# Performance work log

Measured on AMD Instinct MI355X. Metric: run time of the kernel, lower is better.

## Reference

```python
import jax, jax.numpy as jnp
import numpy as np

B, N, D, H, DH, M = 4, 4096, 1024, 16, 64, 256
EPS = 1e-4


def softmax_kernel(data, P, is_query):
    # data: [b,h,n,dh], P: [m,dh]  (FAVOR+ positive softmax features)
    dn = data.shape[-1] ** -0.25
    ratio = P.shape[0] ** -0.5
    dd = jnp.einsum('bhnd,md->bhnm', dn * data, P)
    diag = (jnp.sum(data * data, axis=-1) * 0.5 * dn * dn)[..., None]  # [b,h,n,1]
    if is_query:
        mx = jnp.max(dd, axis=-1, keepdims=True)  # per-query max
    else:
        mx = jnp.max(dd)  # global max (as in torch source)
    return ratio * (jnp.exp(dd - diag - mx) + EPS)


def setup_inputs() -> dict:
    key = jax.random.key(0)
    ks = jax.random.split(key, 6)
    s = 1.0 / np.sqrt(D).astype(np.float32)
    x = jax.random.normal(ks[0], (B, N, D), jnp.float32)
    Wq = jax.random.normal(ks[1], (D, H * DH), jnp.float32) * s
    Wk = jax.random.normal(ks[2], (D, H * DH), jnp.float32) * s
    Wv = jax.random.normal(ks[3], (D, H * DH), jnp.float32) * s
    Wo = jax.random.normal(ks[4], (H * DH, D), jnp.float32) * s
    bo = jnp.zeros((D,), jnp.float32)
    P = jax.random.normal(ks[5], (M, DH), jnp.float32)  # gaussian (orthogonal) projection
    return {'x': x, 'Wq': Wq, 'Wk': Wk, 'Wv': Wv, 'Wo': Wo, 'bo': bo, 'P': P}


def reference(x, Wq, Wk, Wv, Wo, bo, P):
    b, n, _ = x.shape
    # qkv projections, split heads: b n (h d) -> b h n d
    def proj(W):
        return (x @ W).reshape(b, n, H, DH).transpose(0, 2, 1, 3)
    q, k, v = proj(Wq), proj(Wk), proj(Wv)
    qp = softmax_kernel(q, P, is_query=True)   # [b,h,n,m]
    kp = softmax_kernel(k, P, is_query=False)  # [b,h,n,m]
    # linear attention (Performer)
    k_cumsum = kp.sum(axis=-2)                                   # [b,h,m]
    D_inv = 1.0 / jnp.einsum('bhnm,bhm->bhn', qp, k_cumsum)      # [b,h,n]
    ctx = jnp.einsum('bhnm,bhne->bhme', kp, v)                   # [b,h,m,dh]
    out = jnp.einsum('bhme,bhnm,bhn->bhne', ctx, qp, D_inv)      # [b,h,n,dh]
    out = out.transpose(0, 2, 1, 3).reshape(b, n, H * DH)
    return out @ Wo + bo
```

## Files before the change

### kernel.cpp

```cpp
#include <hip/hip_runtime.h>
#include <math.h>

#define NB 4
#define NSEQ 4096
#define DM 1024
#define NHEAD 16
#define DHD 64
#define MF 256
#define ROWS 16384

#define DN 0.35355339059327373f
#define RATIO 0.0625f
#define HALF_DN2 0.0625f
#define EPSF 1.0e-4f
#define THR_DEFER 4.0f

typedef __attribute__((ext_vector_type(4))) float f32x4;
typedef __attribute__((ext_vector_type(8))) short short8;
typedef __attribute__((ext_vector_type(4))) short short4v;
typedef __attribute__((ext_vector_type(8))) __bf16 bf16x8;
typedef unsigned short ushort_t;

__device__ __forceinline__ unsigned short f2bf(float f) {
  unsigned int u = __builtin_bit_cast(unsigned int, f);
  u += 0x7FFFu + ((u >> 16) & 1u);
  return (unsigned short)(u >> 16);
}
__device__ __forceinline__ float bf2f(unsigned short h) {
  unsigned int u = ((unsigned int)h) << 16;
  return __builtin_bit_cast(float, u);
}

__device__ __forceinline__ f32x4 mfma16(short8 a, short8 b, f32x4 c) {
  return __builtin_amdgcn_mfma_f32_16x16x32_bf16(
      __builtin_bit_cast(bf16x8, a), __builtin_bit_cast(bf16x8, b), c, 0, 0, 0);
}

__device__ __forceinline__ f32x4 mfma16x16(short4v a, short4v b, f32x4 c) {
#if __has_builtin(__builtin_amdgcn_mfma_f32_16x16x16bf16_1k)
  return __builtin_amdgcn_mfma_f32_16x16x16bf16_1k(a, b, c, 0, 0, 0);
#elif __has_builtin(__builtin_amdgcn_mfma_f32_16x16x16_bf16)
  typedef __attribute__((ext_vector_type(4))) __bf16 bf16x4;
  return __builtin_amdgcn_mfma_f32_16x16x16_bf16(
      __builtin_bit_cast(bf16x4, a), __builtin_bit_cast(bf16x4, b), c, 0, 0, 0);
#else
  asm volatile("s_nop 1\n\t"
               "v_mfma_f32_16x16x16_bf16 %0, %1, %2, %0\n\t"
               "s_nop 7"
               : "+v"(c) : "v"(a), "v"(b));
  return c;
#endif
}

__device__ __forceinline__ void glds16(const void* g, void* l) {
  __builtin_amdgcn_global_load_lds(
      (const __attribute__((address_space(1))) unsigned int*)g,
      (__attribute__((address_space(3))) unsigned int*)l, 16, 0, 0);
}

__global__ __launch_bounds__(256) void wtrans(const float* __restrict__ W,
                                              ushort_t* __restrict__ Wt)
{
  __shared__ float ts[64][68];
  const int tid = threadIdx.x;
  const int k0 = blockIdx.y * 64, n0 = blockIdx.x * 64;
  const int r = tid >> 4, c4 = (tid & 15) * 4;
  #pragma unroll
  for (int i = 0; i < 4; ++i) {
    float4 v = *(const float4*)&W[(size_t)(k0 + r + i * 16) * DM + n0 + c4];
    *(float4*)&ts[r + i * 16][c4] = v;
  }
  __syncthreads();
  #pragma unroll
  for (int i = 0; i < 4; ++i) {
    const int n = r + i * 16;
    ushort4 o;
    o.x = f2bf(ts[c4 + 0][n]); o.y = f2bf(ts[c4 + 1][n]);
    o.z = f2bf(ts[c4 + 2][n]); o.w = f2bf(ts[c4 + 3][n]);
    *(ushort4*)&Wt[(size_t)(n0 + n) * DM + k0 + c4] = o;
  }
}

__global__ __launch_bounds__(256) void psplit(const float* __restrict__ P,
                                              ushort_t* __restrict__ PHI,
                                              ushort_t* __restrict__ PLO)
{
  const int i = blockIdx.x * 256 + threadIdx.x;
  const float v = P[i];
  const unsigned short h = f2bf(v);
  PHI[i] = h;
  PLO[i] = f2bf(v - bf2f(h));
}

__global__ __launch_bounds__(256) void xconv(const float* __restrict__ x,
                                             ushort_t* __restrict__ xb)
{
  const size_t i = ((size_t)blockIdx.x * 256 + threadIdx.x) * 8;
  const float4 a = *(const float4*)&x[i];
  const float4 c = *(const float4*)&x[i + 4];
  short8 o;
  o[0] = f2bf(a.x); o[1] = f2bf(a.y); o[2] = f2bf(a.z); o[3] = f2bf(a.w);
  o[4] = f2bf(c.x); o[5] = f2bf(c.y); o[6] = f2bf(c.z); o[7] = f2bf(c.w);
  *(short8*)&xb[i] = o;
}

template<int EPI>
__global__ __launch_bounds__(256) void gemm_k(const ushort_t* __restrict__ Ab,
                                              const ushort_t* __restrict__ Bt,
                                              const float* __restrict__ bias,
                                              float* __restrict__ C,
                                              ushort_t* __restrict__ VT,
                                              ushort_t* __restrict__ OHL,
                                              float* __restrict__ DIAG)
{
  constexpr int K = DM, N = DM;
  __shared__ ushort_t As[128 * 32];
  __shared__ ushort_t Bs[128 * 32];

  const int tid = threadIdx.x;
  const int l = tid & 63, w = tid >> 6;
  const int ll = l & 15, lh = l >> 4;
  const int wr = w >> 1, wc = w & 1;

  const int bid = blockIdx.x;
  const int swz = (bid & 7) * ((int)gridDim.x >> 3) + (bid >> 3);
  const int bm = swz >> 3, bn = swz & 7;
  const int row0 = bm * 128, col0 = bn * 128;

  const int pb0 = w * 128 + l, pb1 = pb0 + 64;
  const int brow0 = pb0 >> 2, bkq0 = (pb0 & 3) ^ ((brow0 >> 1) & 3);
  const int brow1 = pb1 >> 2, bkq1 = (pb1 & 3) ^ ((brow1 >> 1) & 3);
  const ushort_t* bsrc0 = Bt + (size_t)(col0 + brow0) * K + bkq0 * 8;
  const ushort_t* bsrc1 = Bt + (size_t)(col0 + brow1) * K + bkq1 * 8;
  ushort_t* bdst0 = &Bs[(size_t)(w * 128) * 8];
  ushort_t* bdst1 = &Bs[(size_t)(w * 128 + 64) * 8];

  const ushort_t* asrc0 = Ab + (size_t)(row0 + brow0) * K + bkq0 * 8;
  const ushort_t* asrc1 = Ab + (size_t)(row0 + brow1) * K + bkq1 * 8;

  int aoff[4], boff[4];
  #pragma unroll
  for (int mt = 0; mt < 4; ++mt) {
    const int r = wr * 64 + mt * 16 + ll;
    aoff[mt] = (r * 4 + (lh ^ ((r >> 1) & 3))) * 8;
  }
  #pragma unroll
  for (int nt = 0; nt < 4; ++nt) {
    const int r = wc * 64 + nt * 16 + ll;
    boff[nt] = (r * 4 + (lh ^ ((r >> 1) & 3))) * 8;
  }

  f32x4 acc[4][4];
  #pragma unroll
  for (int i = 0; i < 4; ++i)
    #pragma unroll
    for (int j = 0; j < 4; ++j) acc[i][j] = (f32x4){0.f, 0.f, 0.f, 0.f};

  for (int k0 = 0; k0 < K; k0 += 32) {
    __syncthreads();
    glds16(asrc0 + k0, &As[(size_t)(w * 128) * 8]);
    glds16(asrc1 + k0, &As[(size_t)(w * 128 + 64) * 8]);
    glds16(bsrc0 + k0, bdst0);
    glds16(bsrc1 + k0, bdst1);
    __syncthreads();

    short8 av[4], bv[4];
    #pragma unroll
    for (int mt = 0; mt < 4; ++mt) av[mt] = *(const short8*)&As[aoff[mt]];
    #pragma unroll
    for (int nt = 0; nt < 4; ++nt) bv[nt] = *(const short8*)&Bs[boff[nt]];
    #pragma unroll
    for (int mt = 0; mt < 4; ++mt)
      #pragma unroll
      for (int nt = 0; nt < 4; ++nt)
        acc[mt][nt] = mfma16(av[mt], bv[nt], acc[mt][nt]);
  }

  if constexpr (EPI == 1) {
    #pragma unroll
    for (int mt = 0; mt < 4; ++mt) {
      #pragma unroll
      for (int nt = 0; nt < 4; ++nt) {
        const int row = row0 + wr * 64 + mt * 16 + lh * 4;
        const int col = col0 + wc * 64 + nt * 16 + ll;
        const float bv_ = bias[col];
        #pragma unroll
        for (int j = 0; j < 4; ++j)
          C[(size_t)(row + j) * N + col] = acc[mt][nt][j] + bv_;
      }
    }
  } else if constexpr (EPI == 2) {
    #pragma unroll
    for (int mt = 0; mt < 4; ++mt) {
      #pragma unroll
      for (int nt = 0; nt < 4; ++nt) {
        const int rg = row0 + wr * 64 + mt * 16 + lh * 4;
        const int cg = col0 + wc * 64 + nt * 16 + ll;
        const int b = rg >> 12, n = rg & 4095;
        const int h = cg >> 6, dh = cg & 63;
        ushort4 o;
        o.x = f2bf(acc[mt][nt][0]); o.y = f2bf(acc[mt][nt][1]);
        o.z = f2bf(acc[mt][nt][2]); o.w = f2bf(acc[mt][nt][3]);
        *(ushort4*)&VT[(((size_t)b * 16 + h) * 64 + dh) * 4096 + n] = o;
      }
    }
  } else {
    const int hglob = (col0 >> 6) + wc;
    #pragma unroll
    for (int mt = 0; mt < 4; ++mt) {
      float rssq[4] = {0.f, 0.f, 0.f, 0.f};
      #pragma unroll
      for (int nt = 0; nt < 4; ++nt) {
        const int row = row0 + wr * 64 + mt * 16 + lh * 4;
        const int e = nt * 16 + ll;
        #pragma unroll
        for (int j = 0; j < 4; ++j) {
          const float v = acc[mt][nt][j];
          rssq[j] += v * v;
          const unsigned short hh = f2bf(v);
          const size_t base = ((size_t)(row + j) * 16 + hglob) * 128 + e;
          OHL[base] = hh;
          OHL[base + 64] = f2bf(v - bf2f(hh));
        }
      }
      #pragma unroll
      for (int j = 0; j < 4; ++j) {
        float s = rssq[j];
        s += __shfl_xor(s, 1, 64); s += __shfl_xor(s, 2, 64);
        s += __shfl_xor(s, 4, 64); s += __shfl_xor(s, 8, 64);
        if (ll == 0) {
          const int row = row0 + wr * 64 + mt * 16 + lh * 4 + j;
          DIAG[(((row >> 12) * 16 + hglob) << 12) + (row & 4095)] = HALF_DN2 * s;
        }
      }
    }
  }
}

__global__ __launch_bounds__(256, 4) void kside6(const ushort_t* __restrict__ KHL,
                                                 const ushort_t* __restrict__ VT,
                                                 const ushort_t* __restrict__ PHI,
                                                 const ushort_t* __restrict__ PLO,
                                                 const float* __restrict__ DIAGK,
                                                 float* __restrict__ partC,
                                                 float* __restrict__ partK,
                                                 float* __restrict__ mw,
                                                 float* __restrict__ vsum,
                                                 unsigned* __restrict__ mxp)
{
  const int tid = threadIdx.x;
  const int l = tid & 63, mg = tid >> 6;
  const int ll = l & 15, lh = l >> 4;
  const int blk = blockIdx.x;
  const int bh = blk >> 4, ck = (blk >> 1) & 7, mh = blk & 1;
  const int b = bh >> 4, h = bh & 15;
  const int mbase = mh * 128 + mg * 32;

  short8 pfh[2][2], pfl[2][2];
  #pragma unroll
  for (int mt = 0; mt < 2; ++mt)
    #pragma unroll
    for (int ks = 0; ks < 2; ++ks) {
      const size_t off = (size_t)(mbase + mt * 16 + ll) * 64 + ks * 32 + lh * 8;
      pfh[mt][ks] = *(const short8*)&PHI[off];
      pfl[mt][ks] = *(const short8*)&PLO[off];
    }

  f32x4 apv[2][4];
  #pragma unroll
  for (int i = 0; i < 2; ++i)
    #pragma unroll
    for (int j = 0; j < 4; ++j) apv[i][j] = (f32x4){0.f, 0.f, 0.f, 0.f};
  float kcp[2] = {0.f, 0.f};
  float vs[4] = {0.f, 0.f, 0.f, 0.f};
  float m_run = -1.0e30f, tmax = -1.0e30f;

  const int n0 = ck * 512;
  const ushort_t* krow = KHL + ((size_t)(b * NSEQ + n0 + ll) * 16 + h) * 128 + lh * 8;
  const ushort_t* vrow = VT + (size_t)bh * 64 * NSEQ + n0 + lh * 4;
  const float* drow = DIAGK + bh * 4096 + n0 + lh * 4;

  for (int it = 0; it < 32; ++it) {
    const ushort_t* kp_ = krow + (size_t)it * 16 * 2048;
    const short8 kh0 = *(const short8*)(kp_);
    const short8 kh1 = *(const short8*)(kp_ + 32);
    const short8 kl0 = *(const short8*)(kp_ + 64);
    const short8 kl1 = *(const short8*)(kp_ + 96);
    const float4 dg4 = *(const float4*)(drow + it * 16);
    short4v vf[4];
    #pragma unroll
    for (int dt = 0; dt < 4; ++dt)
      vf[dt] = *(const short4v*)&vrow[(size_t)(dt * 16 + ll) * NSEQ + it * 16];

    f32x4 dda[2];
    #pragma unroll
    for (int mt = 0; mt < 2; ++mt) {
      f32x4 acc = (f32x4){0.f, 0.f, 0.f, 0.f};
      acc = mfma16(kh0, pfh[mt][0], acc); acc = mfma16(kh1, pfh[mt][1], acc);
      acc = mfma16(kh0, pfl[mt][0], acc); acc = mfma16(kh1, pfl[mt][1], acc);
      acc = mfma16(kl0, pfh[mt][0], acc); acc = mfma16(kl1, pfh[mt][1], acc);
      #pragma unroll
      for (int jr = 0; jr < 4; ++jr) acc[jr] *= DN;
      dda[mt] = acc;
    }

    float pm = -1.0e30f;
    #pragma unroll
    for (int mt = 0; mt < 2; ++mt)
      #pragma unroll
      for (int jr = 0; jr < 4; ++jr) pm = fmaxf(pm, dda[mt][jr]);
    tmax = fmaxf(tmax, pm);
    if (!__all(pm <= m_run + THR_DEFER)) {
      float pw = fmaxf(pm, m_run);
      pw = fmaxf(pw, __shfl_xor(pw, 1, 64));  pw = fmaxf(pw, __shfl_xor(pw, 2, 64));
      pw = fmaxf(pw, __shfl_xor(pw, 4, 64));  pw = fmaxf(pw, __shfl_xor(pw, 8, 64));
      pw = fmaxf(pw, __shfl_xor(pw, 16, 64)); pw = fmaxf(pw, __shfl_xor(pw, 32, 64));
      const float sc = __expf(m_run - pw);
      #pragma unroll
      for (int mt = 0; mt < 2; ++mt) {
        kcp[mt] *= sc;
        #pragma unroll
        for (int dt = 0; dt < 4; ++dt) apv[mt][dt] *= sc;
      }
      m_run = pw;
    }

    const float dgv[4] = {dg4.x, dg4.y, dg4.z, dg4.w};
    short4v qa[2];
    #pragma unroll
    for (int mt = 0; mt < 2; ++mt) {
      short4v o;
      float s = 0.f;
      #pragma unroll
      for (int jr = 0; jr < 4; ++jr) {
        const float kv = __expf(dda[mt][jr] - dgv[jr] - m_run);
        const unsigned short ub = f2bf(kv);
        o[jr] = (short)ub;
        s += bf2f(ub);
      }
      qa[mt] = o;
      kcp[mt] += s;
    }

    if (mh == 0 && mg == 0) {
      #pragma unroll
      for (int dt = 0; dt < 4; ++dt)
        #pragma unroll
        for (int e = 0; e < 4; ++e) vs[dt] += bf2f((ushort_t)vf[dt][e]);
    }

    #pragma unroll
    for (int dt = 0; dt < 4; ++dt)
      #pragma unroll
      for (int mt = 0; mt < 2; ++mt)
        apv[mt][dt] = mfma16x16(qa[mt], vf[dt], apv[mt][dt]);
  }

  #pragma unroll
  for (int mt = 0; mt < 2; ++mt) {
    float s = kcp[mt];
    s += __shfl_xor(s, 16, 64);
    s += __shfl_xor(s, 32, 64);
    if (lh == 0) partK[blk * 128 + mg * 32 + mt * 16 + ll] = s;
  }
  #pragma unroll
  for (int mt = 0; mt < 2; ++mt)
    #pragma unroll
    for (int dt = 0; dt < 4; ++dt)
      #pragma unroll
      for (int jr = 0; jr < 4; ++jr) {
        const int ml = mg * 32 + mt * 16 + lh * 4 + jr;
        const int dh = dt * 16 + ll;
        partC[(size_t)blk * 8192 + (size_t)ml * 64 + dh] = apv[mt][dt][jr];
      }
  if (mh == 0 && mg == 0) {
    #pragma unroll
    for (int dt = 0; dt < 4; ++dt) {
      float s = vs[dt];
      s += __shfl_xor(s, 16, 64);
      s += __shfl_xor(s, 32, 64);
      if (lh == 0) atomicAdd(&vsum[bh * 64 + dt * 16 + ll], s);
    }
  }
  tmax = fmaxf(tmax, __shfl_xor(tmax, 1, 64));  tmax = fmaxf(tmax, __shfl_xor(tmax, 2, 64));
  tmax = fmaxf(tmax, __shfl_xor(tmax, 4, 64));  tmax = fmaxf(tmax, __shfl_xor(tmax, 8, 64));
  tmax = fmaxf(tmax, __shfl_xor(tmax, 16, 64)); tmax = fmaxf(tmax, __shfl_xor(tmax, 32, 64));
  if (l == 0) {
    atomicMax(mxp, __float_as_uint(tmax));
    mw[blk * 4 + mg] = m_run;
  }
}

__global__ __launch_bounds__(256) void combine2(const float* __restrict__ partC,
                                                const float* __restrict__ partK,
                                                const float* __restrict__ mw,
                                                const float* __restrict__ vsum,
                                                const unsigned* __restrict__ mxp,
                                                float* __restrict__ KCS,
                                                ushort_t* __restrict__ CTH,
                                                ushort_t* __restrict__ CTL,
                                                float* __restrict__ CTSUM,
                                                float* __restrict__ KCSSUM)
{
  const int tid = threadIdx.x;
  const int bh = blockIdx.x >> 2, mc = blockIdx.x & 3;
  const int mh = mc >> 1;
  const float MX = __uint_as_float(*mxp);
  float s[8][2];
  #pragma unroll
  for (int c = 0; c < 8; ++c) {
    const int blkc = bh * 16 + c * 2 + mh;
    #pragma unroll
    for (int g = 0; g < 2; ++g)
      s[c][g] = RATIO * __expf(mw[blkc * 4 + (mc & 1) * 2 + g] - MX);
  }

  __shared__ float ts[64][68];
  const int r = tid >> 4, c4 = (tid & 15) * 4;
  const float reps = RATIO * EPSF;
  const float4 v4 = *(const float4*)&vsum[bh * 64 + c4];
  #pragma unroll
  for (int i = 0; i < 4; ++i) {
    const int ml = r + i * 16;
    const int g = ml >> 5;
    const int mloc = (mc & 1) * 64 + ml;
    float4 a;
    a.x = reps * v4.x; a.y = reps * v4.y; a.z = reps * v4.z; a.w = reps * v4.w;
    #pragma unroll
    for (int c = 0; c < 8; ++c) {
      const size_t blkc = bh * 16 + c * 2 + mh;
      const float4 p = *(const float4*)&partC[blkc * 8192 + (size_t)mloc * 64 + c4];
      a.x += s[c][g] * p.x; a.y += s[c][g] * p.y;
      a.z += s[c][g] * p.z; a.w += s[c][g] * p.w;
    }
    *(float4*)&ts[ml][c4] = a;
  }
  if (tid < 64) {
    const int m = mc * 64 + tid;
    const int g = tid >> 5;
    const int mloc = (mc & 1) * 64 + tid;
    float kv = reps * 4096.0f;
    #pragma unroll
    for (int c = 0; c < 8; ++c)
      kv += s[c][g] * partK[(bh * 16 + c * 2 + mh) * 128 + mloc];
    KCS[bh * 256 + m] = kv;
    float ks = kv;
    #pragma unroll
    for (int off = 1; off < 64; off <<= 1) ks += __shfl_xor(ks, off, 64);
    if (tid == 0) atomicAdd(&KCSSUM[bh], ks);
  }
  __syncthreads();
  #pragma unroll
  for (int i = 0; i < 4; ++i) {
    const int dh = r + i * 16;
    ushort4 oh, ol;
    float csum = 0.f;
    #pragma unroll
    for (int k = 0; k < 4; ++k) {
      const float v = ts[c4 + k][dh];
      csum += v;
      const unsigned short hh = f2bf(v);
      ((unsigned short*)&oh)[k] = hh;
      ((unsigned short*)&ol)[k] = f2bf(v - bf2f(hh));
    }
    const size_t o = ((size_t)bh * 64 + dh) * MF + mc * 64 + c4;
    *(ushort4*)&CTH[o] = oh;
    *(ushort4*)&CTL[o] = ol;
    csum += __shfl_xor(csum, 1, 64); csum += __shfl_xor(csum, 2, 64);
    csum += __shfl_xor(csum, 4, 64); csum += __shfl_xor(csum, 8, 64);
    if ((tid & 15) == 0) atomicAdd(&CTSUM[bh * 64 + dh], csum);
  }
}

__global__ __launch_bounds__(512, 2) void qside7(const ushort_t* __restrict__ QHL,
                                                 const ushort_t* __restrict__ PHI,
                                                 const ushort_t* __restrict__ PLO,
                                                 const float* __restrict__ DIAGQ,
                                                 const float* __restrict__ kcs,
                                                 const ushort_t* __restrict__ CTH,
                                                 const ushort_t* __restrict__ CTL,
                                                 const float* __restrict__ CTSUM,
                                                 const float* __restrict__ KCSSUM,
                                                 ushort_t* __restrict__ attb)
{
  extern __shared__ ushort_t lds[];
  ushort_t* pst = lds;
  ushort_t* ctf = lds + 32768;
  ushort_t* kcf = lds + 65536;
  float* ctsum_s = (float*)(lds + 69632);

  const int tid = threadIdx.x;
  const int l = tid & 63, w = tid >> 6;
  const int ll = l & 15, lh = l >> 4;
  const int bh = blockIdx.x >> 4, qt = blockIdx.x & 15;
  const int b = bh >> 4, h = bh & 15;

  #pragma unroll
  for (int i = 0; i < 8; ++i) {
    const int f = tid + i * 512;
    const int fl = f & 63, r = f >> 6;
    const int p = r & 1, ks = (r >> 1) & 1, mt = r >> 2;
    const ushort_t* src = (p ? PLO : PHI) + (mt * 16 + (fl & 15)) * 64 + ks * 32 + (fl >> 4) * 8;
    *(short8*)&pst[f * 8] = *(const short8*)src;
  }
  #pragma unroll
  for (int i = 0; i < 16; ++i) {
    const int g = tid + i * 512;
    const int gl = g & 63, r = g >> 6;
    const int dt = r & 3, r2 = r >> 2, mt = r2 & 15, p = r2 >> 4;
    const ushort_t* src = (p ? CTL : CTH) +
        ((size_t)bh * 64 + dt * 16 + (gl & 15)) * MF + mt * 16 + (gl >> 4) * 4;
    *(ushort4*)&ctf[g * 4] = *(const ushort4*)src;
  }
  #pragma unroll
  for (int i = 0; i < 2; ++i) {
    const int u = tid + i * 512;
    const int ul = u & 63, mt = u >> 6;
    const int cll = ul & 15, clh = ul >> 4;
    ushort4 o = make_ushort4(0, 0, 0, 0);
    if (cll < 2) {
      #pragma unroll
      for (int e = 0; e < 4; ++e) {
        const float kv = kcs[bh * MF + mt * 16 + clh * 4 + e];
        const unsigned short hi = f2bf(kv);
        ((ushort_t*)&o)[e] = (cll == 0) ? hi : f2bf(kv - bf2f(hi));
      }
    }
    *(ushort4*)&kcf[u * 4] = o;
  }
  if (tid < 64) ctsum_s[tid] = CTSUM[bh * 64 + tid];
  const float kcss = KCSSUM[bh];

  const int nloc0 = qt * 256 + w * 32;
  const int rowb0 = b * NSEQ + nloc0;

  short8 qh0[2], ql0[2], qh1[2], ql1[2];
  #pragma unroll
  for (int ks = 0; ks < 2; ++ks) {
    const size_t base = ((size_t)(rowb0 + ll) * 16 + h) * 128 + ks * 32 + lh * 8;
    qh0[ks] = *(const short8*)&QHL[base];
    ql0[ks] = *(const short8*)&QHL[base + 64];
    qh1[ks] = *(const short8*)&QHL[base + (size_t)16 * 2048];
    ql1[ks] = *(const short8*)&QHL[base + (size_t)16 * 2048 + 64];
  }
  const float dg0 = DIAGQ[bh * 4096 + nloc0 + ll];
  const float dg1 = DIAGQ[bh * 4096 + nloc0 + 16 + ll];

  __syncthreads();

  f32x4 av0[4], av1[4];
  #pragma unroll
  for (int dt = 0; dt < 4; ++dt) {
    av0[dt] = (f32x4){0.f, 0.f, 0.f, 0.f};
    av1[dt] = (f32x4){0.f, 0.f, 0.f, 0.f};
  }
  f32x4 aK0 = (f32x4){0.f, 0.f, 0.f, 0.f};
  f32x4 aK1 = (f32x4){0.f, 0.f, 0.f, 0.f};
  float m0 = -1.0e30f, m1 = -1.0e30f, t0 = -1.0e30f, t1 = -1.0e30f;

  for (int mt = 0; mt < 16; ++mt) {
    const short8 ph0 = *(const short8*)&pst[((mt * 2 + 0) * 2 + 0) * 512 + l * 8];
    const short8 ph1 = *(const short8*)&pst[((mt * 2 + 1) * 2 + 0) * 512 + l * 8];
    const short8 pl0 = *(const short8*)&pst[((mt * 2 + 0) * 2 + 1) * 512 + l * 8];
    const short8 pl1 = *(const short8*)&pst[((mt * 2 + 1) * 2 + 1) * 512 + l * 8];
    f32x4 a0 = (f32x4){0.f, 0.f, 0.f, 0.f};
    f32x4 a1 = (f32x4){0.f, 0.f, 0.f, 0.f};
    a0 = mfma16(ph0, qh0[0], a0); a0 = mfma16(ph1, qh0[1], a0);
    a0 = mfma16(ph0, ql0[0], a0); a0 = mfma16(ph1, ql0[1], a0);
    a0 = mfma16(pl0, qh0[0], a0); a0 = mfma16(pl1, qh0[1], a0);
    a1 = mfma16(ph0, qh1[0], a1); a1 = mfma16(ph1, qh1[1], a1);
    a1 = mfma16(ph0, ql1[0], a1); a1 = mfma16(ph1, ql1[1], a1);
    a1 = mfma16(pl0, qh1[0], a1); a1 = mfma16(pl1, qh1[1], a1);
    #pragma unroll
    for (int jr = 0; jr < 4; ++jr) { a0[jr] *= DN; a1[jr] *= DN; }

    const float pm0 = fmaxf(fmaxf(a0[0], a0[1]), fmaxf(a0[2], a0[3]));
    const float pm1 = fmaxf(fmaxf(a1[0], a1[1]), fmaxf(a1[2], a1[3]));
    t0 = fmaxf(t0, pm0);
    t1 = fmaxf(t1, pm1);
    if (!__all((pm0 <= m0 + THR_DEFER) && (pm1 <= m1 + THR_DEFER))) {
      float pw0 = fmaxf(pm0, m0), pw1 = fmaxf(pm1, m1);
      pw0 = fmaxf(pw0, __shfl_xor(pw0, 16, 64)); pw0 = fmaxf(pw0, __shfl_xor(pw0, 32, 64));
      pw1 = fmaxf(pw1, __shfl_xor(pw1, 16, 64)); pw1 = fmaxf(pw1, __shfl_xor(pw1, 32, 64));
      const float sc0l = __expf(m0 - pw0);
      const float sc1l = __expf(m1 - pw1);
      m0 = pw0; m1 = pw1;
      #pragma unroll
      for (int jr = 0; jr < 4; ++jr) {
        const int src = (l & 48) | (lh * 4 + jr);
        const float s0 = __shfl(sc0l, src, 64);
        const float s1 = __shfl(sc1l, src, 64);
        #pragma unroll
        for (int dt = 0; dt < 4; ++dt) { av0[dt][jr] *= s0; av1[dt][jr] *= s1; }
        aK0[jr] *= s0; aK1[jr] *= s1;
      }
    }

    short4v qp0, qp1;
    #pragma unroll
    for (int jr = 0; jr < 4; ++jr) {
      qp0[jr] = (short)f2bf(__expf(a0[jr] - dg0 - m0));
      qp1[jr] = (short)f2bf(__expf(a1[jr] - dg1 - m1));
    }
    const short4v kcv = *(const short4v*)&kcf[mt * 256 + l * 4];
    aK0 = mfma16x16(qp0, kcv, aK0);
    aK1 = mfma16x16(qp1, kcv, aK1);
    #pragma unroll
    for (int dt = 0; dt < 4; ++dt) {
      const short4v ch = *(const short4v*)&ctf[(mt * 4 + dt) * 256 + l * 4];
      const short4v cl = *(const short4v*)&ctf[((16 + mt) * 4 + dt) * 256 + l * 4];
      av0[dt] = mfma16x16(qp0, ch, av0[dt]);
      av0[dt] = mfma16x16(qp0, cl, av0[dt]);
      av1[dt] = mfma16x16(qp1, ch, av1[dt]);
      av1[dt] = mfma16x16(qp1, cl, av1[dt]);
    }
  }

  t0 = fmaxf(t0, __shfl_xor(t0, 16, 64)); t0 = fmaxf(t0, __shfl_xor(t0, 32, 64));
  t1 = fmaxf(t1, __shfl_xor(t1, 16, 64)); t1 = fmaxf(t1, __shfl_xor(t1, 32, 64));

  float e0s[4], e1s[4], di0[4], di1[4];
  #pragma unroll
  for (int jr = 0; jr < 4; ++jr) {
    const int src = (l & 48) | (lh * 4 + jr);
    e0s[jr] = __expf(__shfl(m0, src, 64) - __shfl(t0, src, 64));
    e1s[jr] = __expf(__shfl(m1, src, 64) - __shfl(t1, src, 64));
    const float h0 = __shfl(aK0[jr], (l & 48), 64);
    const float lo0 = __shfl(aK0[jr], (l & 48) | 1, 64);
    const float h1 = __shfl(aK1[jr], (l & 48), 64);
    const float lo1 = __shfl(aK1[jr], (l & 48) | 1, 64);
    di0[jr] = 1.0f / (e0s[jr] * (h0 + lo0) + EPSF * kcss);
    di1[jr] = 1.0f / (e1s[jr] * (h1 + lo1) + EPSF * kcss);
  }

  #pragma unroll
  for (int dt = 0; dt < 4; ++dt) {
    const int col = h * DHD + dt * 16 + ll;
    const float cts = EPSF * ctsum_s[dt * 16 + ll];
    #pragma unroll
    for (int jr = 0; jr < 4; ++jr) {
      const float num0 = e0s[jr] * av0[dt][jr] + cts;
      const float num1 = e1s[jr] * av1[dt][jr] + cts;
      attb[(size_t)(rowb0 + lh * 4 + jr) * DM + col] = f2bf(num0 * di0[jr]);
      attb[(size_t)(rowb0 + 16 + lh * 4 + jr) * DM + col] = f2bf(num1 * di1[jr]);
    }
  }
}

extern "C" void kernel_launch(void* const* d_in, const int* in_sizes, int n_in,
                              void* d_out, int out_size, void* d_ws, size_t ws_size,
                              hipStream_t stream)
{
  const float* x  = (const float*)d_in[0];
  const float* Wq = (const float*)d_in[1];
  const float* Wk = (const float*)d_in[2];
  const float* Wv = (const float*)d_in[3];
  const float* Wo = (const float*)d_in[4];
  const float* bo = (const float*)d_in[5];
  const float* P  = (const float*)d_in[6];
  float* out = (float*)d_out;

  char* wp = (char*)d_ws;
  ushort_t* QHL   = (ushort_t*)(wp + 0);
  ushort_t* KHL   = (ushort_t*)(wp + 67108864);
  ushort_t* VT    = (ushort_t*)(wp + 134217728);
  ushort_t* Wqt   = (ushort_t*)(wp + 167772160);
  ushort_t* Wkt   = (ushort_t*)(wp + 169869312);
  ushort_t* Wvt   = (ushort_t*)(wp + 171966464);
  ushort_t* Wot   = (ushort_t*)(wp + 174063616);
  ushort_t* PHI   = (ushort_t*)(wp + 176160768);
  ushort_t* PLO   = (ushort_t*)(wp + 176193536);
  float*    DIAGQ = (float*)(wp + 176226304);
  float*    DIAGK = (float*)(wp + 177274880);
  float*    PARTK = (float*)(wp + 178323456);
  float*    MW    = (float*)(wp + 178847744);
  float*    VSUM  = (float*)(wp + 178864128);
  unsigned* MX    = (unsigned*)(wp + 178880512);
  float*    CTSUM = (float*)(wp + 178880768);
  float*    KCSSUM= (float*)(wp + 178897152);
  float*    KCS   = (float*)(wp + 178897408);
  ushort_t* CTH   = (ushort_t*)(wp + 178962944);
  ushort_t* CTL   = (ushort_t*)(wp + 181060096);
  ushort_t* ATTB  = KHL;

  float*    PARTC = (float*)d_out;
  ushort_t* XB    = (ushort_t*)((char*)d_out + 33554432);

  dim3 tg(16, 16);
  wtrans<<<tg, 256, 0, stream>>>(Wq, Wqt);
  wtrans<<<tg, 256, 0, stream>>>(Wk, Wkt);
  wtrans<<<tg, 256, 0, stream>>>(Wv, Wvt);
  wtrans<<<tg, 256, 0, stream>>>(Wo, Wot);
  psplit<<<64, 256, 0, stream>>>(P, PHI, PLO);
  xconv<<<8192, 256, 0, stream>>>(x, XB);
  hipMemsetAsync(VSUM, 0, 33280, stream);

  gemm_k<3><<<1024, 256, 0, stream>>>(XB, Wqt, nullptr, nullptr, nullptr, QHL, DIAGQ);
  gemm_k<3><<<1024, 256, 0, stream>>>(XB, Wkt, nullptr, nullptr, nullptr, KHL, DIAGK);
  gemm_k<2><<<1024, 256, 0, stream>>>(XB, Wvt, nullptr, nullptr, VT, nullptr, nullptr);

  kside6<<<1024, 256, 0, stream>>>(KHL, VT, PHI, PLO, DIAGK, PARTC, PARTK, MW, VSUM, MX);
  combine2<<<256, 256, 0, stream>>>(PARTC, PARTK, MW, VSUM, MX, KCS, CTH, CTL, CTSUM, KCSSUM);
  qside7<<<1024, 512, 139520, stream>>>(QHL, PHI, PLO, DIAGQ, KCS, CTH, CTL, CTSUM, KCSSUM, ATTB);

  gemm_k<1><<<1024, 256, 0, stream>>>(ATTB, Wot, bo, out, nullptr, nullptr, nullptr);
}
```

Before: 489.6 us.

## Merge kside m-halves into 512-thread blocks and prefetch next K tile

```diff
diff --git a/kernel.cpp b/kernel.cpp
--- a/kernel.cpp
+++ b/kernel.cpp
@@ -237,7 +237,7 @@
   }
 }
 
-__global__ __launch_bounds__(256, 4) void kside6(const ushort_t* __restrict__ KHL,
+__global__ __launch_bounds__(512, 4) void kside7(const ushort_t* __restrict__ KHL,
                                                  const ushort_t* __restrict__ VT,
                                                  const ushort_t* __restrict__ PHI,
                                                  const ushort_t* __restrict__ PLO,
@@ -252,9 +252,9 @@
   const int l = tid & 63, mg = tid >> 6;
   const int ll = l & 15, lh = l >> 4;
   const int blk = blockIdx.x;
-  const int bh = blk >> 4, ck = (blk >> 1) & 7, mh = blk & 1;
+  const int bh = blk >> 3, ck = blk & 7;
   const int b = bh >> 4, h = bh & 15;
-  const int mbase = mh * 128 + mg * 32;
+  const int mbase = mg * 32;
 
   short8 pfh[2][2], pfl[2][2];
   #pragma unroll
@@ -280,12 +280,19 @@
   const ushort_t* vrow = VT + (size_t)bh * 64 * NSEQ + n0 + lh * 4;
   const float* drow = DIAGK + bh * 4096 + n0 + lh * 4;
 
+  short8 kh0 = *(const short8*)(krow);
+  short8 kh1 = *(const short8*)(krow + 32);
+  short8 kl0 = *(const short8*)(krow + 64);
+  short8 kl1 = *(const short8*)(krow + 96);
+
   for (int it = 0; it < 32; ++it) {
-    const ushort_t* kp_ = krow + (size_t)it * 16 * 2048;
-    const short8 kh0 = *(const short8*)(kp_);
-    const short8 kh1 = *(const short8*)(kp_ + 32);
-    const short8 kl0 = *(const short8*)(kp_ + 64);
-    const short8 kl1 = *(const short8*)(kp_ + 96);
+    const int itn = (it < 31) ? it + 1 : 31;
+    const ushort_t* kpn = krow + (size_t)itn * 16 * 2048;
+    const short8 nh0 = *(const short8*)(kpn);
+    const short8 nh1 = *(const short8*)(kpn + 32);
+    const short8 nl0 = *(const short8*)(kpn + 64);
+    const short8 nl1 = *(const short8*)(kpn + 96);
+
     const float4 dg4 = *(const float4*)(drow + it * 16);
     short4v vf[4];
     #pragma unroll
@@ -342,7 +349,7 @@
       kcp[mt] += s;
     }
 
-    if (mh == 0 && mg == 0) {
+    if (mg == 0) {
       #pragma unroll
       for (int dt = 0; dt < 4; ++dt)
         #pragma unroll
@@ -354,6 +361,8 @@
       #pragma unroll
       for (int mt = 0; mt < 2; ++mt)
         apv[mt][dt] = mfma16x16(qa[mt], vf[dt], apv[mt][dt]);
+
+    kh0 = nh0; kh1 = nh1; kl0 = nl0; kl1 = nl1;
   }
 
   #pragma unroll
@@ -361,7 +370,7 @@
     float s = kcp[mt];
     s += __shfl_xor(s, 16, 64);
     s += __shfl_xor(s, 32, 64);
-    if (lh == 0) partK[blk * 128 + mg * 32 + mt * 16 + ll] = s;
+    if (lh == 0) partK[blk * 256 + mbase + mt * 16 + ll] = s;
   }
   #pragma unroll
   for (int mt = 0; mt < 2; ++mt)
@@ -369,11 +378,11 @@
     for (int dt = 0; dt < 4; ++dt)
       #pragma unroll
       for (int jr = 0; jr < 4; ++jr) {
-        const int ml = mg * 32 + mt * 16 + lh * 4 + jr;
+        const int m = mbase + mt * 16 + lh * 4 + jr;
         const int dh = dt * 16 + ll;
-        partC[(size_t)blk * 8192 + (size_t)ml * 64 + dh] = apv[mt][dt][jr];
-      }
-  if (mh == 0 && mg == 0) {
+        partC[(size_t)blk * 16384 + (size_t)m * 64 + dh] = apv[mt][dt][jr];
+      }
+  if (mg == 0) {
     #pragma unroll
     for (int dt = 0; dt < 4; ++dt) {
       float s = vs[dt];
@@ -387,11 +396,11 @@
   tmax = fmaxf(tmax, __shfl_xor(tmax, 16, 64)); tmax = fmaxf(tmax, __shfl_xor(tmax, 32, 64));
   if (l == 0) {
     atomicMax(mxp, __float_as_uint(tmax));
-    mw[blk * 4 + mg] = m_run;
-  }
-}
-
-__global__ __launch_bounds__(256) void combine2(const float* __restrict__ partC,
+    mw[blk * 8 + mg] = m_run;
+  }
+}
+
+__global__ __launch_bounds__(256) void combine3(const float* __restrict__ partC,
                                                 const float* __restrict__ partK,
                                                 const float* __restrict__ mw,
                                                 const float* __restrict__ vsum,
@@ -404,16 +413,13 @@
 {
   const int tid = threadIdx.x;
   const int bh = blockIdx.x >> 2, mc = blockIdx.x & 3;
-  const int mh = mc >> 1;
   const float MX = __uint_as_float(*mxp);
   float s[8][2];
   #pragma unroll
-  for (int c = 0; c < 8; ++c) {
-    const int blkc = bh * 16 + c * 2 + mh;
+  for (int c = 0; c < 8; ++c)
     #pragma unroll
     for (int g = 0; g < 2; ++g)
-      s[c][g] = RATIO * __expf(mw[blkc * 4 + (mc & 1) * 2 + g] - MX);
-  }
+      s[c][g] = RATIO * __expf(mw[(bh * 8 + c) * 8 + mc * 2 + g] - MX);
 
   __shared__ float ts[64][68];
   const int r = tid >> 4, c4 = (tid & 15) * 4;
@@ -423,13 +429,13 @@
   for (int i = 0; i < 4; ++i) {
     const int ml = r + i * 16;
     const int g = ml >> 5;
-    const int mloc = (mc & 1) * 64 + ml;
+    const int m = mc * 64 + ml;
     float4 a;
     a.x = reps * v4.x; a.y = reps * v4.y; a.z = reps * v4.z; a.w = reps * v4.w;
     #pragma unroll
     for (int c = 0; c < 8; ++c) {
-      const size_t blkc = bh * 16 + c * 2 + mh;
-      const float4 p = *(const float4*)&partC[blkc * 8192 + (size_t)mloc * 64 + c4];
+      const size_t blkc = bh * 8 + c;
+      const float4 p = *(const float4*)&partC[blkc * 16384 + (size_t)m * 64 + c4];
       a.x += s[c][g] * p.x; a.y += s[c][g] * p.y;
       a.z += s[c][g] * p.z; a.w += s[c][g] * p.w;
     }
@@ -438,11 +444,10 @@
   if (tid < 64) {
     const int m = mc * 64 + tid;
     const int g = tid >> 5;
-    const int mloc = (mc & 1) * 64 + tid;
     float kv = reps * 4096.0f;
     #pragma unroll
     for (int c = 0; c < 8; ++c)
-      kv += s[c][g] * partK[(bh * 16 + c * 2 + mh) * 128 + mloc];
+      kv += s[c][g] * partK[(bh * 8 + c) * 256 + m];
     KCS[bh * 256 + m] = kv;
     float ks = kv;
     #pragma unroll
@@ -699,8 +704,8 @@
   gemm_k<3><<<1024, 256, 0, stream>>>(XB, Wkt, nullptr, nullptr, nullptr, KHL, DIAGK);
   gemm_k<2><<<1024, 256, 0, stream>>>(XB, Wvt, nullptr, nullptr, VT, nullptr, nullptr);
 
-  kside6<<<1024, 256, 0, stream>>>(KHL, VT, PHI, PLO, DIAGK, PARTC, PARTK, MW, VSUM, MX);
-  combine2<<<256, 256, 0, stream>>>(PARTC, PARTK, MW, VSUM, MX, KCS, CTH, CTL, CTSUM, KCSSUM);
+  kside7<<<512, 512, 0, stream>>>(KHL, VT, PHI, PLO, DIAGK, PARTC, PARTK, MW, VSUM, MX);
+  combine3<<<256, 256, 0, stream>>>(PARTC, PARTK, MW, VSUM, MX, KCS, CTH, CTL, CTSUM, KCSSUM);
   qside7<<<1024, 512, 139520, stream>>>(QHL, PHI, PLO, DIAGQ, KCS, CTH, CTL, CTSUM, KCSSUM, ATTB);
 
   gemm_k<1><<<1024, 256, 0, stream>>>(ATTB, Wot, bo, out, nullptr, nullptr, nullptr);
```

Result: slower. 512.7 us (+4.7%).
